# Kernel optimization log

Measured on AMD Instinct MI355X. Metric: run time of the kernel, lower is better.

Reference implementation:

```python
import jax, jax.numpy as jnp
import numpy as np

BETA = 0.8
THRESHOLD = 1.0


def spike(u):
    # Heaviside fire (forward only)
    return (u > 0).astype(u.dtype)


def setup_inputs() -> dict:
    key = jax.random.key(0)
    ks = jax.random.split(key, 10)
    B, T, S, H, L, OUT = 256, 1024, 7, 64, 4, 3
    x = jax.random.normal(ks[0], (B, T, S), dtype=jnp.float32)
    hidden_states = jnp.zeros((B, T, L, H), dtype=jnp.float32)
    prev_obs = jax.random.normal(ks[1], (B, T, S), dtype=jnp.float32)
    # fc1: Linear(7 -> 64)
    w1 = jax.random.normal(ks[2], (H, S), dtype=jnp.float32) / np.sqrt(S)
    b1 = jnp.zeros((H,), dtype=jnp.float32)
    # L-1 hidden Linear(64 -> 64)
    w_h = jax.random.normal(ks[3], (L - 1, H, H), dtype=jnp.float32) / np.sqrt(H)
    b_h = jnp.zeros((L - 1, H), dtype=jnp.float32)
    # final Linear(64 -> out_features)
    w_out = jax.random.normal(ks[4], (OUT, H), dtype=jnp.float32) / np.sqrt(H)
    b_out = jnp.zeros((OUT,), dtype=jnp.float32)
    return {"x": x, "hidden_states": hidden_states, "prev_obs": prev_obs,
            "w1": w1, "b1": b1, "w_h": w_h, "b_h": b_h,
            "w_out": w_out, "b_out": b_out}


def reference(x, hidden_states, prev_obs, w1, b1, w_h, b_h, w_out, b_out):
    # DIRECT input encoding: x used as-is; new_prev_obs = x.
    # hidden_states: [B, T, L, H]; only t=0 slice is the initial membrane state.
    mem0 = hidden_states[:, 0]                      # [B, L, H]
    L = w_h.shape[0] + 1
    # fc1 applied to the whole sequence up front (as in the original)
    all_cur = jnp.einsum('bts,hs->bth', x, w1) + b1  # [B, T, H]

    def step(mem, cur):
        # mem: [B, L, H], cur: [B, H]
        for l in range(L):
            m_prev = mem[:, l]
            # snntorch Leaky, reset_mechanism='subtract', reset detached
            reset = jax.lax.stop_gradient((m_prev > THRESHOLD).astype(cur.dtype))
            m_new = BETA * m_prev + cur - reset * THRESHOLD
            spk = spike(m_new - THRESHOLD)
            mem = mem.at[:, l].set(m_new)
            if l < L - 1:
                cur = spk @ w_h[l].T + b_h[l]
            else:
                cur = spk @ w_out.T + b_out
        return mem, (cur, mem)

    xs = jnp.swapaxes(all_cur, 0, 1)                # [T, B, H]
    _, (outs, mems) = jax.lax.scan(step, mem0, xs)
    outputs = jnp.swapaxes(outs, 0, 1)              # [B, T, OUT]
    new_hidden_states = jnp.swapaxes(mems, 0, 1)    # [B, T, L, H]
    return outputs, new_hidden_states, x
```

## Files before the change

### kernel.cpp

```cpp
#include <hip/hip_runtime.h>
#include <cstdint>
#include <cstddef>

#define Bq 256
#define Tq 1024
#define Sq 7
#define Hq 64
#define Lq 4
#define OUTq 3

typedef float vf16 __attribute__((ext_vector_type(16)));

__global__ __launch_bounds__(256, 1) void snn_seq_kernel(
    const float* __restrict__ x,
    const float* __restrict__ hs_in,
    const float* __restrict__ w1,
    const float* __restrict__ b1,
    const float* __restrict__ w_h,
    const float* __restrict__ b_h,
    float* __restrict__ out_mem)
{
    __shared__ unsigned long long lmask[2][Lq];

    const int b = blockIdx.x;
    const int lane = threadIdx.x & 63;
    const int wv = threadIdx.x >> 6;

    float m = hs_in[(((size_t)b * Tq) * Lq + wv) * Hq + lane];
    float* omem = out_mem + ((size_t)b * Tq * Lq + wv) * Hq + lane;

    float w1r[Sq];
    float b1r = 0.0f;
    const float* xrow = x + (size_t)b * Tq * Sq;
    float xv[Sq];
    vf16 W0, W1, W2, W3;
    float bhr = 0.0f;

    if (wv == 0) {
#pragma unroll
        for (int s = 0; s < Sq; ++s) w1r[s] = w1[lane * Sq + s];
        b1r = b1[lane];
#pragma unroll
        for (int s = 0; s < Sq; ++s) xv[s] = xrow[s];
    } else {
        const vf16* wr = (const vf16*)(w_h + ((size_t)((wv - 1) * Hq + lane)) * Hq);
        W0 = wr[0]; W1 = wr[1]; W2 = wr[2]; W3 = wr[3];
        bhr = b_h[(wv - 1) * Hq + lane];
    }

#define DOBLK(Wv, word, base)                                        \
    {                                                                \
        _Pragma("unroll") for (int q = 0; q < 4; ++q)                \
        {                                                            \
            float f0 = ((word >> (base + 4 * q + 0)) & 1u) ? 1.0f : 0.0f; \
            float f1 = ((word >> (base + 4 * q + 1)) & 1u) ? 1.0f : 0.0f; \
            float f2 = ((word >> (base + 4 * q + 2)) & 1u) ? 1.0f : 0.0f; \
            float f3 = ((word >> (base + 4 * q + 3)) & 1u) ? 1.0f : 0.0f; \
            a0 = fmaf(f0, Wv[4 * q + 0], a0);                        \
            a1 = fmaf(f1, Wv[4 * q + 1], a1);                        \
            a2 = fmaf(f2, Wv[4 * q + 2], a2);                        \
            a3 = fmaf(f3, Wv[4 * q + 3], a3);                        \
        }                                                            \
    }

    for (int k = 0; k < Tq + Lq - 1; ++k) {
        if (wv == 0) {
            if (k < Tq) {
                const float* xp = xrow + (size_t)(k < Tq - 1 ? k + 1 : k) * Sq;
                float xn[Sq];
#pragma unroll
                for (int s = 0; s < Sq; ++s) xn[s] = xp[s];

                float cur = b1r;
#pragma unroll
                for (int s = 0; s < Sq; ++s) cur = fmaf(xv[s], w1r[s], cur);

                float rst = (m > 1.0f) ? 1.0f : 0.0f;
                float mn = __fadd_rn(__fmul_rn(0.8f, m), cur);
                mn = __fsub_rn(mn, rst);
                m = mn;
                omem[(size_t)k * (Lq * Hq)] = mn;

                unsigned long long msk = __ballot(mn > 1.0f);
                if (lane == 0) lmask[k & 1][0] = msk;
#pragma unroll
                for (int s = 0; s < Sq; ++s) xv[s] = xn[s];
            }
        } else {
            const int t = k - wv;
            if (t >= 0 && t < Tq) {
                uint2 mr = *((const uint2*)&lmask[(k - 1) & 1][wv - 1]);
                unsigned lo = (unsigned)__builtin_amdgcn_readfirstlane((int)mr.x);
                unsigned hi = (unsigned)__builtin_amdgcn_readfirstlane((int)mr.y);

                float a0 = bhr, a1 = 0.0f, a2 = 0.0f, a3 = 0.0f;
                DOBLK(W0, lo, 0)
                DOBLK(W1, lo, 16)
                DOBLK(W2, hi, 0)
                DOBLK(W3, hi, 16)
                float cur = __fadd_rn(__fadd_rn(a0, a1), __fadd_rn(a2, a3));

                float rst = (m > 1.0f) ? 1.0f : 0.0f;
                float mn = __fadd_rn(__fmul_rn(0.8f, m), cur);
                mn = __fsub_rn(mn, rst);
                m = mn;
                omem[(size_t)t * (Lq * Hq)] = mn;

                if (wv < Lq - 1) {
                    unsigned long long msk = __ballot(mn > 1.0f);
                    if (lane == 0) lmask[k & 1][wv] = msk;
                }
            }
        }
        asm volatile("s_waitcnt lgkmcnt(0)\n\ts_barrier" ::: "memory");
    }
#undef DOBLK
}

__global__ __launch_bounds__(256) void snn_out_kernel(
    const float* __restrict__ mem,
    const float* __restrict__ w_out,
    const float* __restrict__ b_out,
    float* __restrict__ out0)
{
    const long long idx = (long long)blockIdx.x * 16 + (threadIdx.x >> 4);
    const int sub = threadIdx.x & 15;
    if (idx >= (long long)Bq * Tq) return;

    float4 mv = ((const float4*)mem)[(size_t)idx * 64 + 48 + sub];
    float4 s;
    s.x = (mv.x > 1.0f) ? 1.0f : 0.0f;
    s.y = (mv.y > 1.0f) ? 1.0f : 0.0f;
    s.z = (mv.z > 1.0f) ? 1.0f : 0.0f;
    s.w = (mv.w > 1.0f) ? 1.0f : 0.0f;

#pragma unroll
    for (int o = 0; o < OUTq; ++o) {
        float4 wv = ((const float4*)w_out)[o * 16 + sub];
        float v = s.x * wv.x + s.y * wv.y + s.z * wv.z + s.w * wv.w;
#pragma unroll
        for (int off = 8; off > 0; off >>= 1) v += __shfl_xor(v, off, 16);
        if (sub == 0) out0[idx * OUTq + o] = v + b_out[o];
    }
}

__global__ __launch_bounds__(256) void copy_x_kernel(
    const float4* __restrict__ src, float4* __restrict__ dst, int n4)
{
    int i = blockIdx.x * 256 + threadIdx.x;
    if (i < n4) dst[i] = src[i];
}

extern "C" void kernel_launch(void* const* d_in, const int* in_sizes, int n_in,
                              void* d_out, int out_size, void* d_ws, size_t ws_size,
                              hipStream_t stream) {
    const float* x     = (const float*)d_in[0];
    const float* hs_in = (const float*)d_in[1];
    const float* w1    = (const float*)d_in[3];
    const float* b1    = (const float*)d_in[4];
    const float* w_h   = (const float*)d_in[5];
    const float* b_h   = (const float*)d_in[6];
    const float* w_out = (const float*)d_in[7];
    const float* b_out = (const float*)d_in[8];

    float* out0 = (float*)d_out;
    float* out1 = out0 + (size_t)Bq * Tq * OUTq;
    float* out2 = out1 + (size_t)Bq * Tq * Lq * Hq;

    snn_seq_kernel<<<Bq, 256, 0, stream>>>(x, hs_in, w1, b1, w_h, b_h, out1);

    const long long nbt = (long long)Bq * Tq;
    snn_out_kernel<<<(int)(nbt / 16), 256, 0, stream>>>(out1, w_out, b_out, out0);

    const int n4 = Bq * Tq * Sq / 4;
    copy_x_kernel<<<(n4 + 255) / 256, 256, 0, stream>>>((const float4*)x, (float4*)out2, n4);
}
```

Baseline: 1.023 ms.

## Batch eight timesteps per pipeline beat to cut block barriers

Restructures the layer-wavefront pipeline so each wave handles eight consecutive timesteps between barriers. Spike masks for all eight steps go into an enlarged LDS buffer, and the next layer reads them with vector loads. This cuts the barrier count about eightfold and loads x in 16-byte vectors per chunk. In exchange the pipeline fill and drain grow to three chunks of eight steps, and the wave registers hold more x values.

```diff
diff --git a/kernel.cpp b/kernel.cpp
--- a/kernel.cpp
+++ b/kernel.cpp
@@ -8,8 +8,12 @@
 #define Hq 64
 #define Lq 4
 #define OUTq 3
+#define Uq 8
+#define NTB (Tq / Uq)
+#define NBEATS (NTB + Lq - 1)
 
 typedef float vf16 __attribute__((ext_vector_type(16)));
+typedef float vf4 __attribute__((ext_vector_type(4)));
 
 __global__ __launch_bounds__(256, 1) void snn_seq_kernel(
     const float* __restrict__ x,
@@ -20,7 +24,7 @@
     const float* __restrict__ b_h,
     float* __restrict__ out_mem)
 {
-    __shared__ unsigned long long lmask[2][Lq];
+    __shared__ __align__(16) unsigned long long lmask[2][Lq][Uq];
 
     const int b = blockIdx.x;
     const int lane = threadIdx.x & 63;
@@ -32,7 +36,7 @@
     float w1r[Sq];
     float b1r = 0.0f;
     const float* xrow = x + (size_t)b * Tq * Sq;
-    float xv[Sq];
+    vf4 xcur[14];
     vf16 W0, W1, W2, W3;
     float bhr = 0.0f;
 
@@ -40,13 +44,16 @@
 #pragma unroll
         for (int s = 0; s < Sq; ++s) w1r[s] = w1[lane * Sq + s];
         b1r = b1[lane];
+        const vf4* xp4 = (const vf4*)xrow;
 #pragma unroll
-        for (int s = 0; s < Sq; ++s) xv[s] = xrow[s];
+        for (int i = 0; i < 14; ++i) xcur[i] = xp4[i];
     } else {
         const vf16* wr = (const vf16*)(w_h + ((size_t)((wv - 1) * Hq + lane)) * Hq);
         W0 = wr[0]; W1 = wr[1]; W2 = wr[2]; W3 = wr[3];
         bhr = b_h[(wv - 1) * Hq + lane];
     }
+
+#define XC(e) xcur[(e) >> 2][(e) & 3]
 
 #define DOBLK(Wv, word, base)                                        \
     {                                                                \
@@ -63,58 +70,69 @@
         }                                                            \
     }
 
-    for (int k = 0; k < Tq + Lq - 1; ++k) {
+    for (int k = 0; k < NBEATS; ++k) {
         if (wv == 0) {
-            if (k < Tq) {
-                const float* xp = xrow + (size_t)(k < Tq - 1 ? k + 1 : k) * Sq;
-                float xn[Sq];
+            if (k < NTB) {
+                const int kp = (k < NTB - 1) ? k + 1 : k;
+                const vf4* xp4 = (const vf4*)(xrow + (size_t)kp * (Uq * Sq));
+                vf4 xn[14];
 #pragma unroll
-                for (int s = 0; s < Sq; ++s) xn[s] = xp[s];
+                for (int i = 0; i < 14; ++i) xn[i] = xp4[i];
 
-                float cur = b1r;
 #pragma unroll
-                for (int s = 0; s < Sq; ++s) cur = fmaf(xv[s], w1r[s], cur);
-
-                float rst = (m > 1.0f) ? 1.0f : 0.0f;
-                float mn = __fadd_rn(__fmul_rn(0.8f, m), cur);
-                mn = __fsub_rn(mn, rst);
-                m = mn;
-                omem[(size_t)k * (Lq * Hq)] = mn;
-
-                unsigned long long msk = __ballot(mn > 1.0f);
-                if (lane == 0) lmask[k & 1][0] = msk;
+                for (int i = 0; i < Uq; ++i) {
+                    float cur = b1r;
 #pragma unroll
-                for (int s = 0; s < Sq; ++s) xv[s] = xn[s];
+                    for (int s = 0; s < Sq; ++s) cur = fmaf(XC(i * Sq + s), w1r[s], cur);
+                    float rst = (m > 1.0f) ? 1.0f : 0.0f;
+                    float mn = __fadd_rn(__fmul_rn(0.8f, m), cur);
+                    mn = __fsub_rn(mn, rst);
+                    m = mn;
+                    omem[(size_t)(k * Uq + i) * (Lq * Hq)] = mn;
+                    unsigned long long msk = __ballot(mn > 1.0f);
+                    if (lane == 0) lmask[k & 1][0][i] = msk;
+                }
+#pragma unroll
+                for (int i = 0; i < 14; ++i) xcur[i] = xn[i];
             }
         } else {
-            const int t = k - wv;
-            if (t >= 0 && t < Tq) {
-                uint2 mr = *((const uint2*)&lmask[(k - 1) & 1][wv - 1]);
-                unsigned lo = (unsigned)__builtin_amdgcn_readfirstlane((int)mr.x);
-                unsigned hi = (unsigned)__builtin_amdgcn_readfirstlane((int)mr.y);
+            const int tt = k - wv;
+            if (tt >= 0 && tt < NTB) {
+                const uint4* mp = (const uint4*)&lmask[(k - 1) & 1][wv - 1][0];
+                uint4 q0 = mp[0], q1 = mp[1], q2 = mp[2], q3 = mp[3];
+                unsigned mw[16] = {q0.x, q0.y, q0.z, q0.w,
+                                   q1.x, q1.y, q1.z, q1.w,
+                                   q2.x, q2.y, q2.z, q2.w,
+                                   q3.x, q3.y, q3.z, q3.w};
+#pragma unroll
+                for (int i = 0; i < Uq; ++i) {
+                    unsigned lo = (unsigned)__builtin_amdgcn_readfirstlane((int)mw[2 * i + 0]);
+                    unsigned hi = (unsigned)__builtin_amdgcn_readfirstlane((int)mw[2 * i + 1]);
 
-                float a0 = bhr, a1 = 0.0f, a2 = 0.0f, a3 = 0.0f;
-                DOBLK(W0, lo, 0)
-                DOBLK(W1, lo, 16)
-                DOBLK(W2, hi, 0)
-                DOBLK(W3, hi, 16)
-                float cur = __fadd_rn(__fadd_rn(a0, a1), __fadd_rn(a2, a3));
+                    float a0 = bhr, a1 = 0.0f, a2 = 0.0f, a3 = 0.0f;
+                    DOBLK(W0, lo, 0)
+                    DOBLK(W1, lo, 16)
+                    DOBLK(W2, hi, 0)
+                    DOBLK(W3, hi, 16)
+                    float cur = __fadd_rn(__fadd_rn(a0, a1), __fadd_rn(a2, a3));
 
-                float rst = (m > 1.0f) ? 1.0f : 0.0f;
-                float mn = __fadd_rn(__fmul_rn(0.8f, m), cur);
-                mn = __fsub_rn(mn, rst);
-                m = mn;
-                omem[(size_t)t * (Lq * Hq)] = mn;
+                    float rst = (m > 1.0f) ? 1.0f : 0.0f;
+                    float mn = __fadd_rn(__fmul_rn(0.8f, m), cur);
+                    mn = __fsub_rn(mn, rst);
+                    m = mn;
+                    omem[(size_t)(tt * Uq + i) * (Lq * Hq)] = mn;
 
-                if (wv < Lq - 1) {
-                    unsigned long long msk = __ballot(mn > 1.0f);
-                    if (lane == 0) lmask[k & 1][wv] = msk;
+                    if (wv < Lq - 1) {
+                        unsigned long long msk = __ballot(mn > 1.0f);
+                        if (lane == 0) lmask[k & 1][wv][i] = msk;
+                    }
                 }
             }
         }
         asm volatile("s_waitcnt lgkmcnt(0)\n\ts_barrier" ::: "memory");
     }
 #undef DOBLK
+#undef XC
 }
 
 __global__ __launch_bounds__(256) void snn_out_kernel(
```

Result: faster. 935.7 us (-8.5%).
